# Kernel optimization log

Measured on AMD Instinct MI355X. Metric: run time of the kernel, lower is better.

## Reference

```python
import jax, jax.numpy as jnp
import numpy as np

NEG_BIG = -1e9


def setup_inputs() -> dict:
    key = jax.random.key(0)
    ks = jax.random.split(key, 6)
    B, Tq, Tv, D, A = 4, 256, 1024, 512, 128
    inputs = jax.random.normal(ks[0], (B, Tv, D), dtype=jnp.float32)
    context = jax.random.normal(ks[1], (B, Tq, D), dtype=jnp.float32)
    mask = jnp.ones((B, Tv), dtype=jnp.int32)  # 1 = valid position
    scale = 1.0 / np.sqrt(D)
    Wk = jax.random.normal(ks[2], (D, A), dtype=jnp.float32) * scale
    bk = jnp.zeros((A,), dtype=jnp.float32)
    Wq = jax.random.normal(ks[3], (D, A), dtype=jnp.float32) * scale
    bq = jnp.zeros((A,), dtype=jnp.float32)
    attn_v = jax.random.normal(ks[4], (A,), dtype=jnp.float32) * (1.0 / np.sqrt(A))
    return {"inputs": inputs, "context": context, "mask": mask,
            "Wk": Wk, "bk": bk, "Wq": Wq, "bq": bq, "attn_v": attn_v}


def reference(inputs, context, mask, Wk, bk, Wq, bq, attn_v):
    # inputs: [B,Tv,D] (keys/values), context: [B,Tq,D] (queries)
    k = jnp.einsum('bvd,da->bva', inputs, Wk) + bk        # [B,Tv,A]
    q = jnp.einsum('bqd,da->bqa', context, Wq) + bq       # [B,Tq,A]
    # additive (Bahdanau) score: sum_a v_a * tanh(q + k)
    t = jnp.tanh(q[:, :, None, :] + k[:, None, :, :])     # [B,Tq,Tv,A]
    scores = jnp.einsum('bqva,a->bqv', t, attn_v)         # [B,Tq,Tv]
    neg = (1.0 - mask.astype(jnp.float32))[:, None, :] * NEG_BIG
    scores = scores + neg
    attn = jax.nn.softmax(scores, axis=-1)                # [B,Tq,Tv]
    return jnp.einsum('bqv,bvd->bqd', attn, inputs)       # [B,Tq,D]
```

## Files before the change

### kernel.cpp

```cpp
#include <hip/hip_runtime.h>
#include <math.h>

#define B   4
#define TQ  256
#define TV  1024
#define D   512
#define A   128

#define LOG2E     1.4426950408889634f
#define TWO_LOG2E 2.8853900817779268f
#define NEG_BIG_F (-1e9f)

#define QBLK (B * TQ / 8)
#define KBLK (B * TV / 8)

__global__ __launch_bounds__(512, 4) void proj_exp_kernel(
    const float* __restrict__ ctx, const float* __restrict__ inp,
    const float* __restrict__ Wq, const float* __restrict__ bq,
    const float* __restrict__ Wk, const float* __restrict__ bk,
    float* __restrict__ Eq, float* __restrict__ EkT) {
  __shared__ float ps[8][8][A];
  __shared__ float es[A][9];

  bool isQ = blockIdx.x < QBLK;
  const float* X; const float* W; const float* bias; int r0;
  if (isQ) { X = ctx; W = Wq; bias = bq; r0 = blockIdx.x * 8; }
  else     { X = inp; W = Wk; bias = bk; r0 = (blockIdx.x - QBLK) * 8; }

  int tid = threadIdx.x;
  int ap = (tid & 63) * 2;
  int g  = tid >> 6;

  int dbase = __builtin_amdgcn_readfirstlane(g * 64);
  const float* Xr = X + (size_t)r0 * D + dbase;
  const float* Wd = W + (size_t)dbase * A + ap;

  float2 acc[8];
#pragma unroll
  for (int j = 0; j < 8; ++j) acc[j] = make_float2(0.f, 0.f);

#pragma unroll 2
  for (int dd = 0; dd < 64; dd += 4) {
    float2 w0 = *(const float2*)(Wd + (size_t)(dd + 0) * A);
    float2 w1 = *(const float2*)(Wd + (size_t)(dd + 1) * A);
    float2 w2 = *(const float2*)(Wd + (size_t)(dd + 2) * A);
    float2 w3 = *(const float2*)(Wd + (size_t)(dd + 3) * A);
    float4 x[8];
#pragma unroll
    for (int j = 0; j < 8; ++j)
      x[j] = *(const float4*)(Xr + (size_t)j * D + dd);
#pragma unroll
    for (int j = 0; j < 8; ++j) {
      acc[j].x = fmaf(x[j].x, w0.x, acc[j].x);
      acc[j].y = fmaf(x[j].x, w0.y, acc[j].y);
      acc[j].x = fmaf(x[j].y, w1.x, acc[j].x);
      acc[j].y = fmaf(x[j].y, w1.y, acc[j].y);
      acc[j].x = fmaf(x[j].z, w2.x, acc[j].x);
      acc[j].y = fmaf(x[j].z, w2.y, acc[j].y);
      acc[j].x = fmaf(x[j].w, w3.x, acc[j].x);
      acc[j].y = fmaf(x[j].w, w3.y, acc[j].y);
    }
  }

#pragma unroll
  for (int j = 0; j < 8; ++j)
    *(float2*)&ps[j][g][ap] = acc[j];
  __syncthreads();

  int j  = tid >> 6;
  int a2 = (tid & 63) * 2;
  float2 s0 = *(const float2*)&ps[j][0][a2];
  float2 s1 = *(const float2*)&ps[j][1][a2];
  float2 s2 = *(const float2*)&ps[j][2][a2];
  float2 s3 = *(const float2*)&ps[j][3][a2];
  float2 s4 = *(const float2*)&ps[j][4][a2];
  float2 s5 = *(const float2*)&ps[j][5][a2];
  float2 s6 = *(const float2*)&ps[j][6][a2];
  float2 s7 = *(const float2*)&ps[j][7][a2];
  float2 bz = *(const float2*)(bias + a2);
  float2 ev;
  ev.x = __builtin_amdgcn_exp2f(
      ((((s0.x + s1.x) + (s2.x + s3.x)) + ((s4.x + s5.x) + (s6.x + s7.x))) + bz.x) * TWO_LOG2E);
  ev.y = __builtin_amdgcn_exp2f(
      ((((s0.y + s1.y) + (s2.y + s3.y)) + ((s4.y + s5.y) + (s6.y + s7.y))) + bz.y) * TWO_LOG2E);

  if (isQ) {
    *(float2*)(Eq + (size_t)(r0 + j) * A + a2) = ev;
  } else {
    es[a2 + 0][j] = ev.x;
    es[a2 + 1][j] = ev.y;
    __syncthreads();
    int b  = r0 >> 10;
    int v0 = r0 & (TV - 1);
    for (int i = tid; i < A * 8; i += 512) {
      int aa = i >> 3, jj = i & 7;
      EkT[((size_t)b * A + aa) * TV + v0 + jj] = es[aa][jj];
    }
  }
}

__global__ __launch_bounds__(512, 4) void score_softmax_kernel(
    const float* __restrict__ Eq, const float* __restrict__ EkT,
    const float* __restrict__ attn_v, const int* __restrict__ mask,
    float* __restrict__ attn) {
  __shared__ float redA[8], redB[8];
  __shared__ float bc[4];

  int tid = threadIdx.x;
  int v0  = (tid & 63) * 2 + (tid >> 6) * 128;
  int xcd = blockIdx.x & 7;
  int grp = blockIdx.x >> 3;
  int b   = xcd & 3;
  int pair = (xcd >> 2) * 64 + grp;
  int r0  = b * TQ + pair * 2;

  const float* eqA = Eq + (size_t)r0 * A;
  const float* eqB = eqA + A;

  float sumV = 0.f;
#pragma unroll 16
  for (int i = 0; i < A; ++i) sumV += attn_v[i];

  const float* ekb = EkT + (size_t)b * A * TV + v0;
  float2 tA = make_float2(0.f, 0.f);
  float2 tB = make_float2(0.f, 0.f);

  float2 p00 = *(const float2*)(ekb + (size_t)0 * TV);
  float2 p01 = *(const float2*)(ekb + (size_t)1 * TV);
  float2 p02 = *(const float2*)(ekb + (size_t)2 * TV);
  float2 p03 = *(const float2*)(ekb + (size_t)3 * TV);
  float2 p10 = *(const float2*)(ekb + (size_t)4 * TV);
  float2 p11 = *(const float2*)(ekb + (size_t)5 * TV);
  float2 p12 = *(const float2*)(ekb + (size_t)6 * TV);
  float2 p13 = *(const float2*)(ekb + (size_t)7 * TV);

  for (int i = 0; i < A; i += 8) {
    {
      float av0 = attn_v[i + 0], av1 = attn_v[i + 1];
      float av2 = attn_v[i + 2], av3 = attn_v[i + 3];
      float qa0 = eqA[i + 0], qa1 = eqA[i + 1], qa2 = eqA[i + 2], qa3 = eqA[i + 3];
      float qb0 = eqB[i + 0], qb1 = eqB[i + 1], qb2 = eqB[i + 2], qb3 = eqB[i + 3];

      tA.x = fmaf(av0, __builtin_amdgcn_rcpf(fmaf(p00.x, qa0, 1.f)), tA.x);
      tA.y = fmaf(av0, __builtin_amdgcn_rcpf(fmaf(p00.y, qa0, 1.f)), tA.y);
      tB.x = fmaf(av0, __builtin_amdgcn_rcpf(fmaf(p00.x, qb0, 1.f)), tB.x);
      tB.y = fmaf(av0, __builtin_amdgcn_rcpf(fmaf(p00.y, qb0, 1.f)), tB.y);

      tA.x = fmaf(av1, __builtin_amdgcn_rcpf(fmaf(p01.x, qa1, 1.f)), tA.x);
      tA.y = fmaf(av1, __builtin_amdgcn_rcpf(fmaf(p01.y, qa1, 1.f)), tA.y);
      tB.x = fmaf(av1, __builtin_amdgcn_rcpf(fmaf(p01.x, qb1, 1.f)), tB.x);
      tB.y = fmaf(av1, __builtin_amdgcn_rcpf(fmaf(p01.y, qb1, 1.f)), tB.y);

      tA.x = fmaf(av2, __builtin_amdgcn_rcpf(fmaf(p02.x, qa2, 1.f)), tA.x);
      tA.y = fmaf(av2, __builtin_amdgcn_rcpf(fmaf(p02.y, qa2, 1.f)), tA.y);
      tB.x = fmaf(av2, __builtin_amdgcn_rcpf(fmaf(p02.x, qb2, 1.f)), tB.x);
      tB.y = fmaf(av2, __builtin_amdgcn_rcpf(fmaf(p02.y, qb2, 1.f)), tB.y);

      tA.x = fmaf(av3, __builtin_amdgcn_rcpf(fmaf(p03.x, qa3, 1.f)), tA.x);
      tA.y = fmaf(av3, __builtin_amdgcn_rcpf(fmaf(p03.y, qa3, 1.f)), tA.y);
      tB.x = fmaf(av3, __builtin_amdgcn_rcpf(fmaf(p03.x, qb3, 1.f)), tB.x);
      tB.y = fmaf(av3, __builtin_amdgcn_rcpf(fmaf(p03.y, qb3, 1.f)), tB.y);
    }
    p00 = *(const float2*)(ekb + (size_t)(i + 8) * TV);
    p01 = *(const float2*)(ekb + (size_t)(i + 9) * TV);
    p02 = *(const float2*)(ekb + (size_t)(i + 10) * TV);
    p03 = *(const float2*)(ekb + (size_t)(i + 11) * TV);

    {
      float av0 = attn_v[i + 4], av1 = attn_v[i + 5];
      float av2 = attn_v[i + 6], av3 = attn_v[i + 7];
      float qa0 = eqA[i + 4], qa1 = eqA[i + 5], qa2 = eqA[i + 6], qa3 = eqA[i + 7];
      float qb0 = eqB[i + 4], qb1 = eqB[i + 5], qb2 = eqB[i + 6], qb3 = eqB[i + 7];

      tA.x = fmaf(av0, __builtin_amdgcn_rcpf(fmaf(p10.x, qa0, 1.f)), tA.x);
      tA.y = fmaf(av0, __builtin_amdgcn_rcpf(fmaf(p10.y, qa0, 1.f)), tA.y);
      tB.x = fmaf(av0, __builtin_amdgcn_rcpf(fmaf(p10.x, qb0, 1.f)), tB.x);
      tB.y = fmaf(av0, __builtin_amdgcn_rcpf(fmaf(p10.y, qb0, 1.f)), tB.y);

      tA.x = fmaf(av1, __builtin_amdgcn_rcpf(fmaf(p11.x, qa1, 1.f)), tA.x);
      tA.y = fmaf(av1, __builtin_amdgcn_rcpf(fmaf(p11.y, qa1, 1.f)), tA.y);
      tB.x = fmaf(av1, __builtin_amdgcn_rcpf(fmaf(p11.x, qb1, 1.f)), tB.x);
      tB.y = fmaf(av1, __builtin_amdgcn_rcpf(fmaf(p11.y, qb1, 1.f)), tB.y);

      tA.x = fmaf(av2, __builtin_amdgcn_rcpf(fmaf(p12.x, qa2, 1.f)), tA.x);
      tA.y = fmaf(av2, __builtin_amdgcn_rcpf(fmaf(p12.y, qa2, 1.f)), tA.y);
      tB.x = fmaf(av2, __builtin_amdgcn_rcpf(fmaf(p12.x, qb2, 1.f)), tB.x);
      tB.y = fmaf(av2, __builtin_amdgcn_rcpf(fmaf(p12.y, qb2, 1.f)), tB.y);

      tA.x = fmaf(av3, __builtin_amdgcn_rcpf(fmaf(p13.x, qa3, 1.f)), tA.x);
      tA.y = fmaf(av3, __builtin_amdgcn_rcpf(fmaf(p13.y, qa3, 1.f)), tA.y);
      tB.x = fmaf(av3, __builtin_amdgcn_rcpf(fmaf(p13.x, qb3, 1.f)), tB.x);
      tB.y = fmaf(av3, __builtin_amdgcn_rcpf(fmaf(p13.y, qb3, 1.f)), tB.y);
    }
    p10 = *(const float2*)(ekb + (size_t)(i + 12) * TV);
    p11 = *(const float2*)(ekb + (size_t)(i + 13) * TV);
    p12 = *(const float2*)(ekb + (size_t)(i + 14) * TV);
    p13 = *(const float2*)(ekb + (size_t)(i + 15) * TV);
  }

  int2 mk = *(const int2*)(mask + b * TV + v0);
  float mkx = (1.f - (float)mk.x) * NEG_BIG_F;
  float mky = (1.f - (float)mk.y) * NEG_BIG_F;
  float2 sA, sB;
  sA.x = sumV - 2.f * tA.x + mkx;
  sA.y = sumV - 2.f * tA.y + mky;
  sB.x = sumV - 2.f * tB.x + mkx;
  sB.y = sumV - 2.f * tB.y + mky;

  float mA = fmaxf(sA.x, sA.y);
  float mB = fmaxf(sB.x, sB.y);
  for (int off = 32; off > 0; off >>= 1) {
    mA = fmaxf(mA, __shfl_down(mA, off, 64));
    mB = fmaxf(mB, __shfl_down(mB, off, 64));
  }
  int w = tid >> 6;
  if ((tid & 63) == 0) { redA[w] = mA; redB[w] = mB; }
  __syncthreads();
  if (tid == 0) {
    float a = redA[0], bm = redB[0];
#pragma unroll
    for (int i = 1; i < 8; ++i) { a = fmaxf(a, redA[i]); bm = fmaxf(bm, redB[i]); }
    bc[0] = a; bc[1] = bm;
  }
  __syncthreads();
  float MA = bc[0], MB = bc[1];

  float2 eAv, eBv;
  eAv.x = __builtin_amdgcn_exp2f((sA.x - MA) * LOG2E);
  eAv.y = __builtin_amdgcn_exp2f((sA.y - MA) * LOG2E);
  eBv.x = __builtin_amdgcn_exp2f((sB.x - MB) * LOG2E);
  eBv.y = __builtin_amdgcn_exp2f((sB.y - MB) * LOG2E);
  float lA = eAv.x + eAv.y;
  float lB = eBv.x + eBv.y;
  for (int off = 32; off > 0; off >>= 1) {
    lA += __shfl_down(lA, off, 64);
    lB += __shfl_down(lB, off, 64);
  }
  __syncthreads();
  if ((tid & 63) == 0) { redA[w] = lA; redB[w] = lB; }
  __syncthreads();
  if (tid == 0) {
    float a = 0.f, bs = 0.f;
#pragma unroll
    for (int i = 0; i < 8; ++i) { a += redA[i]; bs += redB[i]; }
    bc[2] = a; bc[3] = bs;
  }
  __syncthreads();
  float iA = 1.f / bc[2];
  float iB = 1.f / bc[3];

  *(float2*)(attn + (size_t)r0 * TV + v0) =
      make_float2(eAv.x * iA, eAv.y * iA);
  *(float2*)(attn + (size_t)(r0 + 1) * TV + v0) =
      make_float2(eBv.x * iB, eBv.y * iB);
}

__global__ __launch_bounds__(512, 4) void pv_kernel(
    const float* __restrict__ attn, const float* __restrict__ X,
    float* __restrict__ out) {
  __shared__ float lds[8 * 1024];
  int gsl = blockIdx.x & 15;
  int b   = gsl & 3;
  int dt  = gsl >> 2;
  int qt  = blockIdx.x >> 4;
  int q0  = b * TQ + qt * 8;
  int tid  = threadIdx.x;
  int w    = tid >> 6;
  int lane = tid & 63;
  int col  = lane & 31;
  int qh   = lane >> 5;
  int d0 = dt * 128 + col * 4;

  {
    const float4* src = (const float4*)(attn + (size_t)q0 * TV);
    float4* dst = (float4*)lds;
    for (int i = tid; i < 8 * 256; i += 512) dst[i] = src[i];
  }
  __syncthreads();

  float4 acc[4];
#pragma unroll
  for (int j = 0; j < 4; ++j) acc[j] = make_float4(0.f, 0.f, 0.f, 0.f);

  int vbase = w * 128;
  const float* Xb = X + ((size_t)b * TV + vbase) * D + d0;
  const float* arow = &lds[(qh * 4) * 1024 + vbase];

  float4 xc0 = *(const float4*)(Xb + (size_t)0 * D);
  float4 xc1 = *(const float4*)(Xb + (size_t)1 * D);
  float4 xc2 = *(const float4*)(Xb + (size_t)2 * D);
  float4 xc3 = *(const float4*)(Xb + (size_t)3 * D);

  for (int vi = 0; vi < 128; vi += 4) {
    float4 xn0, xn1, xn2, xn3;
    if (vi < 124) {
      const float* Xn = Xb + (size_t)(vi + 4) * D;
      xn0 = *(const float4*)(Xn + (size_t)0 * D);
      xn1 = *(const float4*)(Xn + (size_t)1 * D);
      xn2 = *(const float4*)(Xn + (size_t)2 * D);
      xn3 = *(const float4*)(Xn + (size_t)3 * D);
    }
#pragma unroll
    for (int j = 0; j < 4; ++j) {
      float4 av = *(const float4*)(arow + j * 1024 + vi);
      acc[j].x = fmaf(av.x, xc0.x, acc[j].x);
      acc[j].y = fmaf(av.x, xc0.y, acc[j].y);
      acc[j].z = fmaf(av.x, xc0.z, acc[j].z);
      acc[j].w = fmaf(av.x, xc0.w, acc[j].w);
      acc[j].x = fmaf(av.y, xc1.x, acc[j].x);
      acc[j].y = fmaf(av.y, xc1.y, acc[j].y);
      acc[j].z = fmaf(av.y, xc1.z, acc[j].z);
      acc[j].w = fmaf(av.y, xc1.w, acc[j].w);
      acc[j].x = fmaf(av.z, xc2.x, acc[j].x);
      acc[j].y = fmaf(av.z, xc2.y, acc[j].y);
      acc[j].z = fmaf(av.z, xc2.z, acc[j].z);
      acc[j].w = fmaf(av.z, xc2.w, acc[j].w);
      acc[j].x = fmaf(av.w, xc3.x, acc[j].x);
      acc[j].y = fmaf(av.w, xc3.y, acc[j].y);
      acc[j].z = fmaf(av.w, xc3.z, acc[j].z);
      acc[j].w = fmaf(av.w, xc3.w, acc[j].w);
    }
    xc0 = xn0; xc1 = xn1; xc2 = xn2; xc3 = xn3;
  }

  __syncthreads();

  {
    float4* pat = (float4*)lds + (size_t)w * 256;
#pragma unroll
    for (int j = 0; j < 4; ++j)
      pat[(qh * 4 + j) * 32 + col] = acc[j];
  }
  __syncthreads();

  if (tid < 256) {
    int row = tid >> 5;
    int c   = tid & 31;
    const float4* p = (const float4*)lds + tid;
    float4 r = p[0];
#pragma unroll
    for (int i = 1; i < 8; ++i) {
      float4 t = p[(size_t)i * 256];
      r.x += t.x; r.y += t.y; r.z += t.z; r.w += t.w;
    }
    *(float4*)(out + (size_t)(q0 + row) * D + dt * 128 + c * 4) = r;
  }
}

extern "C" void kernel_launch(void* const* d_in, const int* in_sizes, int n_in,
                              void* d_out, int out_size, void* d_ws, size_t ws_size,
                              hipStream_t stream) {
  const float* inputs  = (const float*)d_in[0];
  const float* context = (const float*)d_in[1];
  const int*   mask    = (const int*)d_in[2];
  const float* Wk      = (const float*)d_in[3];
  const float* bk      = (const float*)d_in[4];
  const float* Wq      = (const float*)d_in[5];
  const float* bq      = (const float*)d_in[6];
  const float* attn_v  = (const float*)d_in[7];
  float* out = (float*)d_out;

  float* Eq   = (float*)d_ws;
  float* EkT  = Eq + B * TQ * A;
  float* attn = EkT + (size_t)B * A * TV;

  proj_exp_kernel<<<QBLK + KBLK, 512, 0, stream>>>(context, inputs, Wq, bq,
                                                   Wk, bk, Eq, EkT);
  score_softmax_kernel<<<B * TQ / 2, 512, 0, stream>>>(Eq, EkT, attn_v, mask,
                                                       attn);
  pv_kernel<<<512, 512, 0, stream>>>(attn, inputs, out);
}
```

Measured before the change: 136.6 us.

## Fuse projection, score-softmax and PV into one cooperative kernel with grid syncs

```diff
diff --git a/kernel.cpp b/kernel.cpp
--- a/kernel.cpp
+++ b/kernel.cpp
@@ -1,5 +1,8 @@
 #include <hip/hip_runtime.h>
+#include <hip/hip_cooperative_groups.h>
 #include <math.h>
+
+namespace cg = cooperative_groups;
 
 #define B   4
 #define TQ  256
@@ -13,6 +16,384 @@
 
 #define QBLK (B * TQ / 8)
 #define KBLK (B * TV / 8)
+
+__global__ __launch_bounds__(512, 4) void fused_kernel(
+    const float* __restrict__ ctx, const float* __restrict__ inp,
+    const float* __restrict__ Wq, const float* __restrict__ bq,
+    const float* __restrict__ Wk, const float* __restrict__ bk,
+    const float* __restrict__ attn_v, const int* __restrict__ mask,
+    float* __restrict__ Eq, float* __restrict__ EkT,
+    float* __restrict__ attn, float* __restrict__ out) {
+  __shared__ float lds[8 * 1024];
+  __shared__ float es[A][9];
+  __shared__ float redA[8], redB[8];
+  __shared__ float bc[4];
+
+  int tid = threadIdx.x;
+  int g   = tid >> 6;
+  int ap  = (tid & 63) * 2;
+  float (*ps)[8][A] = (float (*)[8][A])lds;
+
+  int dbase = __builtin_amdgcn_readfirstlane(g * 64);
+
+  {
+    int r0 = blockIdx.x * 8;
+    const float* Xr = inp + (size_t)r0 * D + dbase;
+    const float* Wd = Wk + (size_t)dbase * A + ap;
+
+    float2 acc[8];
+#pragma unroll
+    for (int j = 0; j < 8; ++j) acc[j] = make_float2(0.f, 0.f);
+
+#pragma unroll 2
+    for (int dd = 0; dd < 64; dd += 4) {
+      float2 w0 = *(const float2*)(Wd + (size_t)(dd + 0) * A);
+      float2 w1 = *(const float2*)(Wd + (size_t)(dd + 1) * A);
+      float2 w2 = *(const float2*)(Wd + (size_t)(dd + 2) * A);
+      float2 w3 = *(const float2*)(Wd + (size_t)(dd + 3) * A);
+      float4 x[8];
+#pragma unroll
+      for (int j = 0; j < 8; ++j)
+        x[j] = *(const float4*)(Xr + (size_t)j * D + dd);
+#pragma unroll
+      for (int j = 0; j < 8; ++j) {
+        acc[j].x = fmaf(x[j].x, w0.x, acc[j].x);
+        acc[j].y = fmaf(x[j].x, w0.y, acc[j].y);
+        acc[j].x = fmaf(x[j].y, w1.x, acc[j].x);
+        acc[j].y = fmaf(x[j].y, w1.y, acc[j].y);
+        acc[j].x = fmaf(x[j].z, w2.x, acc[j].x);
+        acc[j].y = fmaf(x[j].z, w2.y, acc[j].y);
+        acc[j].x = fmaf(x[j].w, w3.x, acc[j].x);
+        acc[j].y = fmaf(x[j].w, w3.y, acc[j].y);
+      }
+    }
+
+#pragma unroll
+    for (int j = 0; j < 8; ++j)
+      *(float2*)&ps[j][g][ap] = acc[j];
+    __syncthreads();
+
+    int j  = tid >> 6;
+    int a2 = (tid & 63) * 2;
+    float2 s0 = *(const float2*)&ps[j][0][a2];
+    float2 s1 = *(const float2*)&ps[j][1][a2];
+    float2 s2 = *(const float2*)&ps[j][2][a2];
+    float2 s3 = *(const float2*)&ps[j][3][a2];
+    float2 s4 = *(const float2*)&ps[j][4][a2];
+    float2 s5 = *(const float2*)&ps[j][5][a2];
+    float2 s6 = *(const float2*)&ps[j][6][a2];
+    float2 s7 = *(const float2*)&ps[j][7][a2];
+    float2 bz = *(const float2*)(bk + a2);
+    float2 ev;
+    ev.x = __builtin_amdgcn_exp2f(
+        ((((s0.x + s1.x) + (s2.x + s3.x)) + ((s4.x + s5.x) + (s6.x + s7.x))) + bz.x) * TWO_LOG2E);
+    ev.y = __builtin_amdgcn_exp2f(
+        ((((s0.y + s1.y) + (s2.y + s3.y)) + ((s4.y + s5.y) + (s6.y + s7.y))) + bz.y) * TWO_LOG2E);
+
+    es[a2 + 0][j] = ev.x;
+    es[a2 + 1][j] = ev.y;
+    __syncthreads();
+
+    int b  = r0 >> 10;
+    int v0 = r0 & (TV - 1);
+    for (int i = tid; i < A * 8; i += 512) {
+      int aa = i >> 3, jj = i & 7;
+      EkT[((size_t)b * A + aa) * TV + v0 + jj] = es[aa][jj];
+    }
+  }
+
+  {
+    int r0 = blockIdx.x * 2;
+    const float* Xr = ctx + (size_t)r0 * D + dbase;
+    const float* Wd = Wq + (size_t)dbase * A + ap;
+
+    float2 a0 = make_float2(0.f, 0.f);
+    float2 a1 = make_float2(0.f, 0.f);
+
+#pragma unroll 4
+    for (int dd = 0; dd < 64; dd += 4) {
+      float2 w0 = *(const float2*)(Wd + (size_t)(dd + 0) * A);
+      float2 w1 = *(const float2*)(Wd + (size_t)(dd + 1) * A);
+      float2 w2 = *(const float2*)(Wd + (size_t)(dd + 2) * A);
+      float2 w3 = *(const float2*)(Wd + (size_t)(dd + 3) * A);
+      float4 x0 = *(const float4*)(Xr + (size_t)0 * D + dd);
+      float4 x1 = *(const float4*)(Xr + (size_t)1 * D + dd);
+      a0.x = fmaf(x0.x, w0.x, a0.x);  a0.y = fmaf(x0.x, w0.y, a0.y);
+      a0.x = fmaf(x0.y, w1.x, a0.x);  a0.y = fmaf(x0.y, w1.y, a0.y);
+      a0.x = fmaf(x0.z, w2.x, a0.x);  a0.y = fmaf(x0.z, w2.y, a0.y);
+      a0.x = fmaf(x0.w, w3.x, a0.x);  a0.y = fmaf(x0.w, w3.y, a0.y);
+      a1.x = fmaf(x1.x, w0.x, a1.x);  a1.y = fmaf(x1.x, w0.y, a1.y);
+      a1.x = fmaf(x1.y, w1.x, a1.x);  a1.y = fmaf(x1.y, w1.y, a1.y);
+      a1.x = fmaf(x1.z, w2.x, a1.x);  a1.y = fmaf(x1.z, w2.y, a1.y);
+      a1.x = fmaf(x1.w, w3.x, a1.x);  a1.y = fmaf(x1.w, w3.y, a1.y);
+    }
+
+    *(float2*)&ps[0][g][ap] = a0;
+    *(float2*)&ps[1][g][ap] = a1;
+    __syncthreads();
+
+    if (tid < 128) {
+      int j  = tid >> 6;
+      int a2 = (tid & 63) * 2;
+      float2 s0 = *(const float2*)&ps[j][0][a2];
+      float2 s1 = *(const float2*)&ps[j][1][a2];
+      float2 s2 = *(const float2*)&ps[j][2][a2];
+      float2 s3 = *(const float2*)&ps[j][3][a2];
+      float2 s4 = *(const float2*)&ps[j][4][a2];
+      float2 s5 = *(const float2*)&ps[j][5][a2];
+      float2 s6 = *(const float2*)&ps[j][6][a2];
+      float2 s7 = *(const float2*)&ps[j][7][a2];
+      float2 bz = *(const float2*)(bq + a2);
+      float2 ev;
+      ev.x = __builtin_amdgcn_exp2f(
+          ((((s0.x + s1.x) + (s2.x + s3.x)) + ((s4.x + s5.x) + (s6.x + s7.x))) + bz.x) * TWO_LOG2E);
+      ev.y = __builtin_amdgcn_exp2f(
+          ((((s0.y + s1.y) + (s2.y + s3.y)) + ((s4.y + s5.y) + (s6.y + s7.y))) + bz.y) * TWO_LOG2E);
+      *(float2*)(Eq + (size_t)(r0 + j) * A + a2) = ev;
+    }
+  }
+
+  cg::this_grid().sync();
+
+  {
+    int v0  = (tid & 63) * 2 + (tid >> 6) * 128;
+    int xcd = blockIdx.x & 7;
+    int grp = blockIdx.x >> 3;
+    int b   = xcd & 3;
+    int pair = (xcd >> 2) * 64 + grp;
+    int r0  = b * TQ + pair * 2;
+
+    const float* eqA = Eq + (size_t)r0 * A;
+    const float* eqB = eqA + A;
+
+    float sumV = 0.f;
+#pragma unroll 16
+    for (int i = 0; i < A; ++i) sumV += attn_v[i];
+
+    const float* ekb = EkT + (size_t)b * A * TV + v0;
+    float2 tA = make_float2(0.f, 0.f);
+    float2 tB = make_float2(0.f, 0.f);
+
+    float2 p00 = *(const float2*)(ekb + (size_t)0 * TV);
+    float2 p01 = *(const float2*)(ekb + (size_t)1 * TV);
+    float2 p02 = *(const float2*)(ekb + (size_t)2 * TV);
+    float2 p03 = *(const float2*)(ekb + (size_t)3 * TV);
+    float2 p10 = *(const float2*)(ekb + (size_t)4 * TV);
+    float2 p11 = *(const float2*)(ekb + (size_t)5 * TV);
+    float2 p12 = *(const float2*)(ekb + (size_t)6 * TV);
+    float2 p13 = *(const float2*)(ekb + (size_t)7 * TV);
+
+    for (int i = 0; i < A; i += 8) {
+      {
+        float av0 = attn_v[i + 0], av1 = attn_v[i + 1];
+        float av2 = attn_v[i + 2], av3 = attn_v[i + 3];
+        float qa0 = eqA[i + 0], qa1 = eqA[i + 1], qa2 = eqA[i + 2], qa3 = eqA[i + 3];
+        float qb0 = eqB[i + 0], qb1 = eqB[i + 1], qb2 = eqB[i + 2], qb3 = eqB[i + 3];
+
+        tA.x = fmaf(av0, __builtin_amdgcn_rcpf(fmaf(p00.x, qa0, 1.f)), tA.x);
+        tA.y = fmaf(av0, __builtin_amdgcn_rcpf(fmaf(p00.y, qa0, 1.f)), tA.y);
+        tB.x = fmaf(av0, __builtin_amdgcn_rcpf(fmaf(p00.x, qb0, 1.f)), tB.x);
+        tB.y = fmaf(av0, __builtin_amdgcn_rcpf(fmaf(p00.y, qb0, 1.f)), tB.y);
+
+        tA.x = fmaf(av1, __builtin_amdgcn_rcpf(fmaf(p01.x, qa1, 1.f)), tA.x);
+        tA.y = fmaf(av1, __builtin_amdgcn_rcpf(fmaf(p01.y, qa1, 1.f)), tA.y);
+        tB.x = fmaf(av1, __builtin_amdgcn_rcpf(fmaf(p01.x, qb1, 1.f)), tB.x);
+        tB.y = fmaf(av1, __builtin_amdgcn_rcpf(fmaf(p01.y, qb1, 1.f)), tB.y);
+
+        tA.x = fmaf(av2, __builtin_amdgcn_rcpf(fmaf(p02.x, qa2, 1.f)), tA.x);
+        tA.y = fmaf(av2, __builtin_amdgcn_rcpf(fmaf(p02.y, qa2, 1.f)), tA.y);
+        tB.x = fmaf(av2, __builtin_amdgcn_rcpf(fmaf(p02.x, qb2, 1.f)), tB.x);
+        tB.y = fmaf(av2, __builtin_amdgcn_rcpf(fmaf(p02.y, qb2, 1.f)), tB.y);
+
+        tA.x = fmaf(av3, __builtin_amdgcn_rcpf(fmaf(p03.x, qa3, 1.f)), tA.x);
+        tA.y = fmaf(av3, __builtin_amdgcn_rcpf(fmaf(p03.y, qa3, 1.f)), tA.y);
+        tB.x = fmaf(av3, __builtin_amdgcn_rcpf(fmaf(p03.x, qb3, 1.f)), tB.x);
+        tB.y = fmaf(av3, __builtin_amdgcn_rcpf(fmaf(p03.y, qb3, 1.f)), tB.y);
+      }
+      p00 = *(const float2*)(ekb + (size_t)(i + 8) * TV);
+      p01 = *(const float2*)(ekb + (size_t)(i + 9) * TV);
+      p02 = *(const float2*)(ekb + (size_t)(i + 10) * TV);
+      p03 = *(const float2*)(ekb + (size_t)(i + 11) * TV);
+
+      {
+        float av0 = attn_v[i + 4], av1 = attn_v[i + 5];
+        float av2 = attn_v[i + 6], av3 = attn_v[i + 7];
+        float qa0 = eqA[i + 4], qa1 = eqA[i + 5], qa2 = eqA[i + 6], qa3 = eqA[i + 7];
+        float qb0 = eqB[i + 4], qb1 = eqB[i + 5], qb2 = eqB[i + 6], qb3 = eqB[i + 7];
+
+        tA.x = fmaf(av0, __builtin_amdgcn_rcpf(fmaf(p10.x, qa0, 1.f)), tA.x);
+        tA.y = fmaf(av0, __builtin_amdgcn_rcpf(fmaf(p10.y, qa0, 1.f)), tA.y);
+        tB.x = fmaf(av0, __builtin_amdgcn_rcpf(fmaf(p10.x, qb0, 1.f)), tB.x);
+        tB.y = fmaf(av0, __builtin_amdgcn_rcpf(fmaf(p10.y, qb0, 1.f)), tB.y);
+
+        tA.x = fmaf(av1, __builtin_amdgcn_rcpf(fmaf(p11.x, qa1, 1.f)), tA.x);
+        tA.y = fmaf(av1, __builtin_amdgcn_rcpf(fmaf(p11.y, qa1, 1.f)), tA.y);
+        tB.x = fmaf(av1, __builtin_amdgcn_rcpf(fmaf(p11.x, qb1, 1.f)), tB.x);
+        tB.y = fmaf(av1, __builtin_amdgcn_rcpf(fmaf(p11.y, qb1, 1.f)), tB.y);
+
+        tA.x = fmaf(av2, __builtin_amdgcn_rcpf(fmaf(p12.x, qa2, 1.f)), tA.x);
+        tA.y = fmaf(av2, __builtin_amdgcn_rcpf(fmaf(p12.y, qa2, 1.f)), tA.y);
+        tB.x = fmaf(av2, __builtin_amdgcn_rcpf(fmaf(p12.x, qb2, 1.f)), tB.x);
+        tB.y = fmaf(av2, __builtin_amdgcn_rcpf(fmaf(p12.y, qb2, 1.f)), tB.y);
+
+        tA.x = fmaf(av3, __builtin_amdgcn_rcpf(fmaf(p13.x, qa3, 1.f)), tA.x);
+        tA.y = fmaf(av3, __builtin_amdgcn_rcpf(fmaf(p13.y, qa3, 1.f)), tA.y);
+        tB.x = fmaf(av3, __builtin_amdgcn_rcpf(fmaf(p13.x, qb3, 1.f)), tB.x);
+        tB.y = fmaf(av3, __builtin_amdgcn_rcpf(fmaf(p13.y, qb3, 1.f)), tB.y);
+      }
+      p10 = *(const float2*)(ekb + (size_t)(i + 12) * TV);
+      p11 = *(const float2*)(ekb + (size_t)(i + 13) * TV);
+      p12 = *(const float2*)(ekb + (size_t)(i + 14) * TV);
+      p13 = *(const float2*)(ekb + (size_t)(i + 15) * TV);
+    }
+
+    int2 mk = *(const int2*)(mask + b * TV + v0);
+    float mkx = (1.f - (float)mk.x) * NEG_BIG_F;
+    float mky = (1.f - (float)mk.y) * NEG_BIG_F;
+    float2 sA, sB;
+    sA.x = sumV - 2.f * tA.x + mkx;
+    sA.y = sumV - 2.f * tA.y + mky;
+    sB.x = sumV - 2.f * tB.x + mkx;
+    sB.y = sumV - 2.f * tB.y + mky;
+
+    float mA = fmaxf(sA.x, sA.y);
+    float mB = fmaxf(sB.x, sB.y);
+    for (int off = 32; off > 0; off >>= 1) {
+      mA = fmaxf(mA, __shfl_down(mA, off, 64));
+      mB = fmaxf(mB, __shfl_down(mB, off, 64));
+    }
+    int w = tid >> 6;
+    if ((tid & 63) == 0) { redA[w] = mA; redB[w] = mB; }
+    __syncthreads();
+    if (tid == 0) {
+      float a = redA[0], bm = redB[0];
+#pragma unroll
+      for (int i = 1; i < 8; ++i) { a = fmaxf(a, redA[i]); bm = fmaxf(bm, redB[i]); }
+      bc[0] = a; bc[1] = bm;
+    }
+    __syncthreads();
+    float MA = bc[0], MB = bc[1];
+
+    float2 eAv, eBv;
+    eAv.x = __builtin_amdgcn_exp2f((sA.x - MA) * LOG2E);
+    eAv.y = __builtin_amdgcn_exp2f((sA.y - MA) * LOG2E);
+    eBv.x = __builtin_amdgcn_exp2f((sB.x - MB) * LOG2E);
+    eBv.y = __builtin_amdgcn_exp2f((sB.y - MB) * LOG2E);
+    float lA = eAv.x + eAv.y;
+    float lB = eBv.x + eBv.y;
+    for (int off = 32; off > 0; off >>= 1) {
+      lA += __shfl_down(lA, off, 64);
+      lB += __shfl_down(lB, off, 64);
+    }
+    __syncthreads();
+    if ((tid & 63) == 0) { redA[w] = lA; redB[w] = lB; }
+    __syncthreads();
+    if (tid == 0) {
+      float a = 0.f, bs = 0.f;
+#pragma unroll
+      for (int i = 0; i < 8; ++i) { a += redA[i]; bs += redB[i]; }
+      bc[2] = a; bc[3] = bs;
+    }
+    __syncthreads();
+    float iA = 1.f / bc[2];
+    float iB = 1.f / bc[3];
+
+    *(float2*)(attn + (size_t)r0 * TV + v0) =
+        make_float2(eAv.x * iA, eAv.y * iA);
+    *(float2*)(attn + (size_t)(r0 + 1) * TV + v0) =
+        make_float2(eBv.x * iB, eBv.y * iB);
+  }
+
+  cg::this_grid().sync();
+
+  {
+    int gsl = blockIdx.x & 15;
+    int b   = gsl & 3;
+    int dt  = gsl >> 2;
+    int qt  = blockIdx.x >> 4;
+    int q0  = b * TQ + qt * 8;
+    int w    = tid >> 6;
+    int lane = tid & 63;
+    int col  = lane & 31;
+    int qh   = lane >> 5;
+    int d0 = dt * 128 + col * 4;
+
+    {
+      const float4* src = (const float4*)(attn + (size_t)q0 * TV);
+      float4* dst = (float4*)lds;
+      for (int i = tid; i < 8 * 256; i += 512) dst[i] = src[i];
+    }
+    __syncthreads();
+
+    float4 acc[4];
+#pragma unroll
+    for (int j = 0; j < 4; ++j) acc[j] = make_float4(0.f, 0.f, 0.f, 0.f);
+
+    int vbase = w * 128;
+    const float* Xb = inp + ((size_t)b * TV + vbase) * D + d0;
+    const float* arow = &lds[(qh * 4) * 1024 + vbase];
+
+    float4 xc0 = *(const float4*)(Xb + (size_t)0 * D);
+    float4 xc1 = *(const float4*)(Xb + (size_t)1 * D);
+    float4 xc2 = *(const float4*)(Xb + (size_t)2 * D);
+    float4 xc3 = *(const float4*)(Xb + (size_t)3 * D);
+
+    for (int vi = 0; vi < 128; vi += 4) {
+      float4 xn0, xn1, xn2, xn3;
+      if (vi < 124) {
+        const float* Xn = Xb + (size_t)(vi + 4) * D;
+        xn0 = *(const float4*)(Xn + (size_t)0 * D);
+        xn1 = *(const float4*)(Xn + (size_t)1 * D);
+        xn2 = *(const float4*)(Xn + (size_t)2 * D);
+        xn3 = *(const float4*)(Xn + (size_t)3 * D);
+      }
+#pragma unroll
+      for (int j = 0; j < 4; ++j) {
+        float4 av = *(const float4*)(arow + j * 1024 + vi);
+        acc[j].x = fmaf(av.x, xc0.x, acc[j].x);
+        acc[j].y = fmaf(av.x, xc0.y, acc[j].y);
+        acc[j].z = fmaf(av.x, xc0.z, acc[j].z);
+        acc[j].w = fmaf(av.x, xc0.w, acc[j].w);
+        acc[j].x = fmaf(av.y, xc1.x, acc[j].x);
+        acc[j].y = fmaf(av.y, xc1.y, acc[j].y);
+        acc[j].z = fmaf(av.y, xc1.z, acc[j].z);
+        acc[j].w = fmaf(av.y, xc1.w, acc[j].w);
+        acc[j].x = fmaf(av.z, xc2.x, acc[j].x);
+        acc[j].y = fmaf(av.z, xc2.y, acc[j].y);
+        acc[j].z = fmaf(av.z, xc2.z, acc[j].z);
+        acc[j].w = fmaf(av.z, xc2.w, acc[j].w);
+        acc[j].x = fmaf(av.w, xc3.x, acc[j].x);
+        acc[j].y = fmaf(av.w, xc3.y, acc[j].y);
+        acc[j].z = fmaf(av.w, xc3.z, acc[j].z);
+        acc[j].w = fmaf(av.w, xc3.w, acc[j].w);
+      }
+      xc0 = xn0; xc1 = xn1; xc2 = xn2; xc3 = xn3;
+    }
+
+    __syncthreads();
+
+    {
+      float4* pat = (float4*)lds + (size_t)w * 256;
+#pragma unroll
+      for (int j = 0; j < 4; ++j)
+        pat[(qh * 4 + j) * 32 + col] = acc[j];
+    }
+    __syncthreads();
+
+    if (tid < 256) {
+      int row = tid >> 5;
+      int c   = tid & 31;
+      const float4* p = (const float4*)lds + tid;
+      float4 r = p[0];
+#pragma unroll
+      for (int i = 1; i < 8; ++i) {
+        float4 t = p[(size_t)i * 256];
+        r.x += t.x; r.y += t.y; r.z += t.z; r.w += t.w;
+      }
+      *(float4*)(out + (size_t)(q0 + row) * D + dt * 128 + c * 4) = r;
+    }
+  }
+}
 
 __global__ __launch_bounds__(512, 4) void proj_exp_kernel(
     const float* __restrict__ ctx, const float* __restrict__ inp,
@@ -125,77 +506,45 @@
   float2 tA = make_float2(0.f, 0.f);
   float2 tB = make_float2(0.f, 0.f);
 
-  float2 p00 = *(const float2*)(ekb + (size_t)0 * TV);
-  float2 p01 = *(const float2*)(ekb + (size_t)1 * TV);
-  float2 p02 = *(const float2*)(ekb + (size_t)2 * TV);
-  float2 p03 = *(const float2*)(ekb + (size_t)3 * TV);
-  float2 p10 = *(const float2*)(ekb + (size_t)4 * TV);
-  float2 p11 = *(const float2*)(ekb + (size_t)5 * TV);
-  float2 p12 = *(const float2*)(ekb + (size_t)6 * TV);
-  float2 p13 = *(const float2*)(ekb + (size_t)7 * TV);
-
-  for (int i = 0; i < A; i += 8) {
-    {
-      float av0 = attn_v[i + 0], av1 = attn_v[i + 1];
-      float av2 = attn_v[i + 2], av3 = attn_v[i + 3];
-      float qa0 = eqA[i + 0], qa1 = eqA[i + 1], qa2 = eqA[i + 2], qa3 = eqA[i + 3];
-      float qb0 = eqB[i + 0], qb1 = eqB[i + 1], qb2 = eqB[i + 2], qb3 = eqB[i + 3];
-
-      tA.x = fmaf(av0, __builtin_amdgcn_rcpf(fmaf(p00.x, qa0, 1.f)), tA.x);
-      tA.y = fmaf(av0, __builtin_amdgcn_rcpf(fmaf(p00.y, qa0, 1.f)), tA.y);
-      tB.x = fmaf(av0, __builtin_amdgcn_rcpf(fmaf(p00.x, qb0, 1.f)), tB.x);
-      tB.y = fmaf(av0, __builtin_amdgcn_rcpf(fmaf(p00.y, qb0, 1.f)), tB.y);
-
-      tA.x = fmaf(av1, __builtin_amdgcn_rcpf(fmaf(p01.x, qa1, 1.f)), tA.x);
-      tA.y = fmaf(av1, __builtin_amdgcn_rcpf(fmaf(p01.y, qa1, 1.f)), tA.y);
-      tB.x = fmaf(av1, __builtin_amdgcn_rcpf(fmaf(p01.x, qb1, 1.f)), tB.x);
-      tB.y = fmaf(av1, __builtin_amdgcn_rcpf(fmaf(p01.y, qb1, 1.f)), tB.y);
-
-      tA.x = fmaf(av2, __builtin_amdgcn_rcpf(fmaf(p02.x, qa2, 1.f)), tA.x);
-      tA.y = fmaf(av2, __builtin_amdgcn_rcpf(fmaf(p02.y, qa2, 1.f)), tA.y);
-      tB.x = fmaf(av2, __builtin_amdgcn_rcpf(fmaf(p02.x, qb2, 1.f)), tB.x);
-      tB.y = fmaf(av2, __builtin_amdgcn_rcpf(fmaf(p02.y, qb2, 1.f)), tB.y);
-
-      tA.x = fmaf(av3, __builtin_amdgcn_rcpf(fmaf(p03.x, qa3, 1.f)), tA.x);
-      tA.y = fmaf(av3, __builtin_amdgcn_rcpf(fmaf(p03.y, qa3, 1.f)), tA.y);
-      tB.x = fmaf(av3, __builtin_amdgcn_rcpf(fmaf(p03.x, qb3, 1.f)), tB.x);
-      tB.y = fmaf(av3, __builtin_amdgcn_rcpf(fmaf(p03.y, qb3, 1.f)), tB.y);
-    }
-    p00 = *(const float2*)(ekb + (size_t)(i + 8) * TV);
-    p01 = *(const float2*)(ekb + (size_t)(i + 9) * TV);
-    p02 = *(const float2*)(ekb + (size_t)(i + 10) * TV);
-    p03 = *(const float2*)(ekb + (size_t)(i + 11) * TV);
-
-    {
-      float av0 = attn_v[i + 4], av1 = attn_v[i + 5];
-      float av2 = attn_v[i + 6], av3 = attn_v[i + 7];
-      float qa0 = eqA[i + 4], qa1 = eqA[i + 5], qa2 = eqA[i + 6], qa3 = eqA[i + 7];
-      float qb0 = eqB[i + 4], qb1 = eqB[i + 5], qb2 = eqB[i + 6], qb3 = eqB[i + 7];
-
-      tA.x = fmaf(av0, __builtin_amdgcn_rcpf(fmaf(p10.x, qa0, 1.f)), tA.x);
-      tA.y = fmaf(av0, __builtin_amdgcn_rcpf(fmaf(p10.y, qa0, 1.f)), tA.y);
-      tB.x = fmaf(av0, __builtin_amdgcn_rcpf(fmaf(p10.x, qb0, 1.f)), tB.x);
-      tB.y = fmaf(av0, __builtin_amdgcn_rcpf(fmaf(p10.y, qb0, 1.f)), tB.y);
-
-      tA.x = fmaf(av1, __builtin_amdgcn_rcpf(fmaf(p11.x, qa1, 1.f)), tA.x);
-      tA.y = fmaf(av1, __builtin_amdgcn_rcpf(fmaf(p11.y, qa1, 1.f)), tA.y);
-      tB.x = fmaf(av1, __builtin_amdgcn_rcpf(fmaf(p11.x, qb1, 1.f)), tB.x);
-      tB.y = fmaf(av1, __builtin_amdgcn_rcpf(fmaf(p11.y, qb1, 1.f)), tB.y);
-
-      tA.x = fmaf(av2, __builtin_amdgcn_rcpf(fmaf(p12.x, qa2, 1.f)), tA.x);
-      tA.y = fmaf(av2, __builtin_amdgcn_rcpf(fmaf(p12.y, qa2, 1.f)), tA.y);
-      tB.x = fmaf(av2, __builtin_amdgcn_rcpf(fmaf(p12.x, qb2, 1.f)), tB.x);
-      tB.y = fmaf(av2, __builtin_amdgcn_rcpf(fmaf(p12.y, qb2, 1.f)), tB.y);
-
-      tA.x = fmaf(av3, __builtin_amdgcn_rcpf(fmaf(p13.x, qa3, 1.f)), tA.x);
-      tA.y = fmaf(av3, __builtin_amdgcn_rcpf(fmaf(p13.y, qa3, 1.f)), tA.y);
-      tB.x = fmaf(av3, __builtin_amdgcn_rcpf(fmaf(p13.x, qb3, 1.f)), tB.x);
-      tB.y = fmaf(av3, __builtin_amdgcn_rcpf(fmaf(p13.y, qb3, 1.f)), tB.y);
-    }
-    p10 = *(const float2*)(ekb + (size_t)(i + 12) * TV);
-    p11 = *(const float2*)(ekb + (size_t)(i + 13) * TV);
-    p12 = *(const float2*)(ekb + (size_t)(i + 14) * TV);
-    p13 = *(const float2*)(ekb + (size_t)(i + 15) * TV);
+  float2 c0 = *(const float2*)(ekb + (size_t)0 * TV);
+  float2 c1 = *(const float2*)(ekb + (size_t)1 * TV);
+  float2 c2 = *(const float2*)(ekb + (size_t)2 * TV);
+  float2 c3 = *(const float2*)(ekb + (size_t)3 * TV);
+
+  for (int i = 0; i < A; i += 4) {
+    float2 n0, n1, n2, n3;
+    if (i < A - 4) {
+      n0 = *(const float2*)(ekb + (size_t)(i + 4) * TV);
+      n1 = *(const float2*)(ekb + (size_t)(i + 5) * TV);
+      n2 = *(const float2*)(ekb + (size_t)(i + 6) * TV);
+      n3 = *(const float2*)(ekb + (size_t)(i + 7) * TV);
+    }
+    float av0 = attn_v[i + 0], av1 = attn_v[i + 1];
+    float av2 = attn_v[i + 2], av3 = attn_v[i + 3];
+    float qa0 = eqA[i + 0], qa1 = eqA[i + 1], qa2 = eqA[i + 2], qa3 = eqA[i + 3];
+    float qb0 = eqB[i + 0], qb1 = eqB[i + 1], qb2 = eqB[i + 2], qb3 = eqB[i + 3];
+
+    tA.x = fmaf(av0, __builtin_amdgcn_rcpf(fmaf(c0.x, qa0, 1.f)), tA.x);
+    tA.y = fmaf(av0, __builtin_amdgcn_rcpf(fmaf(c0.y, qa0, 1.f)), tA.y);
+    tB.x = fmaf(av0, __builtin_amdgcn_rcpf(fmaf(c0.x, qb0, 1.f)), tB.x);
+    tB.y = fmaf(av0, __builtin_amdgcn_rcpf(fmaf(c0.y, qb0, 1.f)), tB.y);
+
+    tA.x = fmaf(av1, __builtin_amdgcn_rcpf(fmaf(c1.x, qa1, 1.f)), tA.x);
+    tA.y = fmaf(av1, __builtin_amdgcn_rcpf(fmaf(c1.y, qa1, 1.f)), tA.y);
+    tB.x = fmaf(av1, __builtin_amdgcn_rcpf(fmaf(c1.x, qb1, 1.f)), tB.x);
+    tB.y = fmaf(av1, __builtin_amdgcn_rcpf(fmaf(c1.y, qb1, 1.f)), tB.y);
+
+    tA.x = fmaf(av2, __builtin_amdgcn_rcpf(fmaf(c2.x, qa2, 1.f)), tA.x);
+    tA.y = fmaf(av2, __builtin_amdgcn_rcpf(fmaf(c2.y, qa2, 1.f)), tA.y);
+    tB.x = fmaf(av2, __builtin_amdgcn_rcpf(fmaf(c2.x, qb2, 1.f)), tB.x);
+    tB.y = fmaf(av2, __builtin_amdgcn_rcpf(fmaf(c2.y, qb2, 1.f)), tB.y);
+
+    tA.x = fmaf(av3, __builtin_amdgcn_rcpf(fmaf(c3.x, qa3, 1.f)), tA.x);
+    tA.y = fmaf(av3, __builtin_amdgcn_rcpf(fmaf(c3.y, qa3, 1.f)), tA.y);
+    tB.x = fmaf(av3, __builtin_amdgcn_rcpf(fmaf(c3.x, qb3, 1.f)), tB.x);
+    tB.y = fmaf(av3, __builtin_amdgcn_rcpf(fmaf(c3.y, qb3, 1.f)), tB.y);
+
+    c0 = n0; c1 = n1; c2 = n2; c3 = n3;
   }
 
   int2 mk = *(const int2*)(mask + b * TV + v0);
@@ -364,9 +713,18 @@
   float* EkT  = Eq + B * TQ * A;
   float* attn = EkT + (size_t)B * A * TV;
 
-  proj_exp_kernel<<<QBLK + KBLK, 512, 0, stream>>>(context, inputs, Wq, bq,
-                                                   Wk, bk, Eq, EkT);
-  score_softmax_kernel<<<B * TQ / 2, 512, 0, stream>>>(Eq, EkT, attn_v, mask,
-                                                       attn);
-  pv_kernel<<<512, 512, 0, stream>>>(attn, inputs, out);
+  void* args[] = {(void*)&context, (void*)&inputs,
+                  (void*)&Wq, (void*)&bq, (void*)&Wk, (void*)&bk,
+                  (void*)&attn_v, (void*)&mask,
+                  (void*)&Eq, (void*)&EkT, (void*)&attn, (void*)&out};
+  hipError_t err = hipLaunchCooperativeKernel(
+      (const void*)fused_kernel, dim3(512), dim3(512), args, 0, stream);
+
+  if (err != hipSuccess) {
+    proj_exp_kernel<<<QBLK + KBLK, 512, 0, stream>>>(context, inputs, Wq, bq,
+                                                     Wk, bk, Eq, EkT);
+    score_softmax_kernel<<<B * TQ / 2, 512, 0, stream>>>(Eq, EkT, attn_v, mask,
+                                                         attn);
+    pv_kernel<<<512, 512, 0, stream>>>(attn, inputs, out);
+  }
 }
```

Measured after the change: 274.4 us. 2.01x slower.

## Score four query rows per block and read attn directly in PV kernel

Applied to the files above, without the earlier changes.

```diff
diff --git a/kernel.cpp b/kernel.cpp
--- a/kernel.cpp
+++ b/kernel.cpp
@@ -99,160 +99,114 @@
   }
 }
 
-__global__ __launch_bounds__(512, 4) void score_softmax_kernel(
+__global__ __launch_bounds__(1024, 4) void score_softmax_kernel(
     const float* __restrict__ Eq, const float* __restrict__ EkT,
     const float* __restrict__ attn_v, const int* __restrict__ mask,
     float* __restrict__ attn) {
-  __shared__ float redA[8], redB[8];
-  __shared__ float bc[4];
+  __shared__ float red[4][16];
+  __shared__ float bc[8];
 
   int tid = threadIdx.x;
-  int v0  = (tid & 63) * 2 + (tid >> 6) * 128;
+  int v0  = tid;
   int xcd = blockIdx.x & 7;
-  int grp = blockIdx.x >> 3;
   int b   = xcd & 3;
-  int pair = (xcd >> 2) * 64 + grp;
-  int r0  = b * TQ + pair * 2;
-
-  const float* eqA = Eq + (size_t)r0 * A;
-  const float* eqB = eqA + A;
+  int quad = (xcd >> 2) * 32 + (blockIdx.x >> 3);
+  int r0  = b * TQ + quad * 4;
+
+  const float* eq0 = Eq + (size_t)(r0 + 0) * A;
+  const float* eq1 = Eq + (size_t)(r0 + 1) * A;
+  const float* eq2 = Eq + (size_t)(r0 + 2) * A;
+  const float* eq3 = Eq + (size_t)(r0 + 3) * A;
 
   float sumV = 0.f;
 #pragma unroll 16
   for (int i = 0; i < A; ++i) sumV += attn_v[i];
 
   const float* ekb = EkT + (size_t)b * A * TV + v0;
-  float2 tA = make_float2(0.f, 0.f);
-  float2 tB = make_float2(0.f, 0.f);
-
-  float2 p00 = *(const float2*)(ekb + (size_t)0 * TV);
-  float2 p01 = *(const float2*)(ekb + (size_t)1 * TV);
-  float2 p02 = *(const float2*)(ekb + (size_t)2 * TV);
-  float2 p03 = *(const float2*)(ekb + (size_t)3 * TV);
-  float2 p10 = *(const float2*)(ekb + (size_t)4 * TV);
-  float2 p11 = *(const float2*)(ekb + (size_t)5 * TV);
-  float2 p12 = *(const float2*)(ekb + (size_t)6 * TV);
-  float2 p13 = *(const float2*)(ekb + (size_t)7 * TV);
-
-  for (int i = 0; i < A; i += 8) {
-    {
-      float av0 = attn_v[i + 0], av1 = attn_v[i + 1];
-      float av2 = attn_v[i + 2], av3 = attn_v[i + 3];
-      float qa0 = eqA[i + 0], qa1 = eqA[i + 1], qa2 = eqA[i + 2], qa3 = eqA[i + 3];
-      float qb0 = eqB[i + 0], qb1 = eqB[i + 1], qb2 = eqB[i + 2], qb3 = eqB[i + 3];
-
-      tA.x = fmaf(av0, __builtin_amdgcn_rcpf(fmaf(p00.x, qa0, 1.f)), tA.x);
-      tA.y = fmaf(av0, __builtin_amdgcn_rcpf(fmaf(p00.y, qa0, 1.f)), tA.y);
-      tB.x = fmaf(av0, __builtin_amdgcn_rcpf(fmaf(p00.x, qb0, 1.f)), tB.x);
-      tB.y = fmaf(av0, __builtin_amdgcn_rcpf(fmaf(p00.y, qb0, 1.f)), tB.y);
-
-      tA.x = fmaf(av1, __builtin_amdgcn_rcpf(fmaf(p01.x, qa1, 1.f)), tA.x);
-      tA.y = fmaf(av1, __builtin_amdgcn_rcpf(fmaf(p01.y, qa1, 1.f)), tA.y);
-      tB.x = fmaf(av1, __builtin_amdgcn_rcpf(fmaf(p01.x, qb1, 1.f)), tB.x);
-      tB.y = fmaf(av1, __builtin_amdgcn_rcpf(fmaf(p01.y, qb1, 1.f)), tB.y);
-
-      tA.x = fmaf(av2, __builtin_amdgcn_rcpf(fmaf(p02.x, qa2, 1.f)), tA.x);
-      tA.y = fmaf(av2, __builtin_amdgcn_rcpf(fmaf(p02.y, qa2, 1.f)), tA.y);
-      tB.x = fmaf(av2, __builtin_amdgcn_rcpf(fmaf(p02.x, qb2, 1.f)), tB.x);
-      tB.y = fmaf(av2, __builtin_amdgcn_rcpf(fmaf(p02.y, qb2, 1.f)), tB.y);
-
-      tA.x = fmaf(av3, __builtin_amdgcn_rcpf(fmaf(p03.x, qa3, 1.f)), tA.x);
-      tA.y = fmaf(av3, __builtin_amdgcn_rcpf(fmaf(p03.y, qa3, 1.f)), tA.y);
-      tB.x = fmaf(av3, __builtin_amdgcn_rcpf(fmaf(p03.x, qb3, 1.f)), tB.x);
-      tB.y = fmaf(av3, __builtin_amdgcn_rcpf(fmaf(p03.y, qb3, 1.f)), tB.y);
-    }
-    p00 = *(const float2*)(ekb + (size_t)(i + 8) * TV);
-    p01 = *(const float2*)(ekb + (size_t)(i + 9) * TV);
-    p02 = *(const float2*)(ekb + (size_t)(i + 10) * TV);
-    p03 = *(const float2*)(ekb + (size_t)(i + 11) * TV);
-
-    {
-      float av0 = attn_v[i + 4], av1 = attn_v[i + 5];
-      float av2 = attn_v[i + 6], av3 = attn_v[i + 7];
-      float qa0 = eqA[i + 4], qa1 = eqA[i + 5], qa2 = eqA[i + 6], qa3 = eqA[i + 7];
-      float qb0 = eqB[i + 4], qb1 = eqB[i + 5], qb2 = eqB[i + 6], qb3 = eqB[i + 7];
-
-      tA.x = fmaf(av0, __builtin_amdgcn_rcpf(fmaf(p10.x, qa0, 1.f)), tA.x);
-      tA.y = fmaf(av0, __builtin_amdgcn_rcpf(fmaf(p10.y, qa0, 1.f)), tA.y);
-      tB.x = fmaf(av0, __builtin_amdgcn_rcpf(fmaf(p10.x, qb0, 1.f)), tB.x);
-      tB.y = fmaf(av0, __builtin_amdgcn_rcpf(fmaf(p10.y, qb0, 1.f)), tB.y);
-
-      tA.x = fmaf(av1, __builtin_amdgcn_rcpf(fmaf(p11.x, qa1, 1.f)), tA.x);
-      tA.y = fmaf(av1, __builtin_amdgcn_rcpf(fmaf(p11.y, qa1, 1.f)), tA.y);
-      tB.x = fmaf(av1, __builtin_amdgcn_rcpf(fmaf(p11.x, qb1, 1.f)), tB.x);
-      tB.y = fmaf(av1, __builtin_amdgcn_rcpf(fmaf(p11.y, qb1, 1.f)), tB.y);
-
-      tA.x = fmaf(av2, __builtin_amdgcn_rcpf(fmaf(p12.x, qa2, 1.f)), tA.x);
-      tA.y = fmaf(av2, __builtin_amdgcn_rcpf(fmaf(p12.y, qa2, 1.f)), tA.y);
-      tB.x = fmaf(av2, __builtin_amdgcn_rcpf(fmaf(p12.x, qb2, 1.f)), tB.x);
-      tB.y = fmaf(av2, __builtin_amdgcn_rcpf(fmaf(p12.y, qb2, 1.f)), tB.y);
-
-      tA.x = fmaf(av3, __builtin_amdgcn_rcpf(fmaf(p13.x, qa3, 1.f)), tA.x);
-      tA.y = fmaf(av3, __builtin_amdgcn_rcpf(fmaf(p13.y, qa3, 1.f)), tA.y);
-      tB.x = fmaf(av3, __builtin_amdgcn_rcpf(fmaf(p13.x, qb3, 1.f)), tB.x);
-      tB.y = fmaf(av3, __builtin_amdgcn_rcpf(fmaf(p13.y, qb3, 1.f)), tB.y);
-    }
-    p10 = *(const float2*)(ekb + (size_t)(i + 12) * TV);
-    p11 = *(const float2*)(ekb + (size_t)(i + 13) * TV);
-    p12 = *(const float2*)(ekb + (size_t)(i + 14) * TV);
-    p13 = *(const float2*)(ekb + (size_t)(i + 15) * TV);
-  }
-
-  int2 mk = *(const int2*)(mask + b * TV + v0);
-  float mkx = (1.f - (float)mk.x) * NEG_BIG_F;
-  float mky = (1.f - (float)mk.y) * NEG_BIG_F;
-  float2 sA, sB;
-  sA.x = sumV - 2.f * tA.x + mkx;
-  sA.y = sumV - 2.f * tA.y + mky;
-  sB.x = sumV - 2.f * tB.x + mkx;
-  sB.y = sumV - 2.f * tB.y + mky;
-
-  float mA = fmaxf(sA.x, sA.y);
-  float mB = fmaxf(sB.x, sB.y);
+  float t[4] = {0.f, 0.f, 0.f, 0.f};
+
+  float c[4], n[4];
+#pragma unroll
+  for (int aa = 0; aa < 4; ++aa) c[aa] = ekb[(size_t)aa * TV];
+
+  for (int i = 0; i < A; i += 4) {
+    if (i < A - 4) {
+#pragma unroll
+      for (int aa = 0; aa < 4; ++aa) n[aa] = ekb[(size_t)(i + 4 + aa) * TV];
+    }
+#pragma unroll
+    for (int aa = 0; aa < 4; ++aa) {
+      float av = attn_v[i + aa];
+      float q0v = eq0[i + aa], q1v = eq1[i + aa];
+      float q2v = eq2[i + aa], q3v = eq3[i + aa];
+      t[0] = fmaf(av, __builtin_amdgcn_rcpf(fmaf(c[aa], q0v, 1.f)), t[0]);
+      t[1] = fmaf(av, __builtin_amdgcn_rcpf(fmaf(c[aa], q1v, 1.f)), t[1]);
+      t[2] = fmaf(av, __builtin_amdgcn_rcpf(fmaf(c[aa], q2v, 1.f)), t[2]);
+      t[3] = fmaf(av, __builtin_amdgcn_rcpf(fmaf(c[aa], q3v, 1.f)), t[3]);
+    }
+#pragma unroll
+    for (int aa = 0; aa < 4; ++aa) c[aa] = n[aa];
+  }
+
+  int mk = mask[b * TV + v0];
+  float mkv = (1.f - (float)mk) * NEG_BIG_F;
+  float s[4];
+#pragma unroll
+  for (int r = 0; r < 4; ++r) s[r] = sumV - 2.f * t[r] + mkv;
+
+  float m[4];
+#pragma unroll
+  for (int r = 0; r < 4; ++r) m[r] = s[r];
   for (int off = 32; off > 0; off >>= 1) {
-    mA = fmaxf(mA, __shfl_down(mA, off, 64));
-    mB = fmaxf(mB, __shfl_down(mB, off, 64));
+#pragma unroll
+    for (int r = 0; r < 4; ++r) m[r] = fmaxf(m[r], __shfl_down(m[r], off, 64));
   }
   int w = tid >> 6;
-  if ((tid & 63) == 0) { redA[w] = mA; redB[w] = mB; }
-  __syncthreads();
-  if (tid == 0) {
-    float a = redA[0], bm = redB[0];
-#pragma unroll
-    for (int i = 1; i < 8; ++i) { a = fmaxf(a, redA[i]); bm = fmaxf(bm, redB[i]); }
-    bc[0] = a; bc[1] = bm;
-  }
-  __syncthreads();
-  float MA = bc[0], MB = bc[1];
-
-  float2 eAv, eBv;
-  eAv.x = __builtin_amdgcn_exp2f((sA.x - MA) * LOG2E);
-  eAv.y = __builtin_amdgcn_exp2f((sA.y - MA) * LOG2E);
-  eBv.x = __builtin_amdgcn_exp2f((sB.x - MB) * LOG2E);
-  eBv.y = __builtin_amdgcn_exp2f((sB.y - MB) * LOG2E);
-  float lA = eAv.x + eAv.y;
-  float lB = eBv.x + eBv.y;
+  if ((tid & 63) == 0) {
+#pragma unroll
+    for (int r = 0; r < 4; ++r) red[r][w] = m[r];
+  }
+  __syncthreads();
+  if (tid < 4) {
+    float a = red[tid][0];
+#pragma unroll
+    for (int i = 1; i < 16; ++i) a = fmaxf(a, red[tid][i]);
+    bc[tid] = a;
+  }
+  __syncthreads();
+  float M0 = bc[0], M1 = bc[1], M2 = bc[2], M3 = bc[3];
+
+  float e[4];
+  e[0] = __builtin_amdgcn_exp2f((s[0] - M0) * LOG2E);
+  e[1] = __builtin_amdgcn_exp2f((s[1] - M1) * LOG2E);
+  e[2] = __builtin_amdgcn_exp2f((s[2] - M2) * LOG2E);
+  e[3] = __builtin_amdgcn_exp2f((s[3] - M3) * LOG2E);
+  float l[4];
+#pragma unroll
+  for (int r = 0; r < 4; ++r) l[r] = e[r];
   for (int off = 32; off > 0; off >>= 1) {
-    lA += __shfl_down(lA, off, 64);
-    lB += __shfl_down(lB, off, 64);
-  }
-  __syncthreads();
-  if ((tid & 63) == 0) { redA[w] = lA; redB[w] = lB; }
-  __syncthreads();
-  if (tid == 0) {
-    float a = 0.f, bs = 0.f;
-#pragma unroll
-    for (int i = 0; i < 8; ++i) { a += redA[i]; bs += redB[i]; }
-    bc[2] = a; bc[3] = bs;
-  }
-  __syncthreads();
-  float iA = 1.f / bc[2];
-  float iB = 1.f / bc[3];
-
-  *(float2*)(attn + (size_t)r0 * TV + v0) =
-      make_float2(eAv.x * iA, eAv.y * iA);
-  *(float2*)(attn + (size_t)(r0 + 1) * TV + v0) =
-      make_float2(eBv.x * iB, eBv.y * iB);
+#pragma unroll
+    for (int r = 0; r < 4; ++r) l[r] += __shfl_down(l[r], off, 64);
+  }
+  __syncthreads();
+  if ((tid & 63) == 0) {
+#pragma unroll
+    for (int r = 0; r < 4; ++r) red[r][w] = l[r];
+  }
+  __syncthreads();
+  if (tid < 4) {
+    float a = 0.f;
+#pragma unroll
+    for (int i = 0; i < 16; ++i) a += red[tid][i];
+    bc[4 + tid] = a;
+  }
+  __syncthreads();
+  float i0 = 1.f / bc[4], i1 = 1.f / bc[5], i2 = 1.f / bc[6], i3 = 1.f / bc[7];
+
+  attn[(size_t)(r0 + 0) * TV + v0] = e[0] * i0;
+  attn[(size_t)(r0 + 1) * TV + v0] = e[1] * i1;
+  attn[(size_t)(r0 + 2) * TV + v0] = e[2] * i2;
+  attn[(size_t)(r0 + 3) * TV + v0] = e[3] * i3;
 }
 
 __global__ __launch_bounds__(512, 4) void pv_kernel(
@@ -271,25 +225,22 @@
   int qh   = lane >> 5;
   int d0 = dt * 128 + col * 4;
 
-  {
-    const float4* src = (const float4*)(attn + (size_t)q0 * TV);
-    float4* dst = (float4*)lds;
-    for (int i = tid; i < 8 * 256; i += 512) dst[i] = src[i];
-  }
-  __syncthreads();
-
   float4 acc[4];
 #pragma unroll
   for (int j = 0; j < 4; ++j) acc[j] = make_float4(0.f, 0.f, 0.f, 0.f);
 
   int vbase = w * 128;
   const float* Xb = X + ((size_t)b * TV + vbase) * D + d0;
-  const float* arow = &lds[(qh * 4) * 1024 + vbase];
+  const float* arow = attn + (size_t)(q0 + qh * 4) * TV + vbase;
 
   float4 xc0 = *(const float4*)(Xb + (size_t)0 * D);
   float4 xc1 = *(const float4*)(Xb + (size_t)1 * D);
   float4 xc2 = *(const float4*)(Xb + (size_t)2 * D);
   float4 xc3 = *(const float4*)(Xb + (size_t)3 * D);
+  float4 ac[4], an[4];
+#pragma unroll
+  for (int j = 0; j < 4; ++j)
+    ac[j] = *(const float4*)(arow + (size_t)j * TV);
 
   for (int vi = 0; vi < 128; vi += 4) {
     float4 xn0, xn1, xn2, xn3;
@@ -299,10 +250,13 @@
       xn1 = *(const float4*)(Xn + (size_t)1 * D);
       xn2 = *(const float4*)(Xn + (size_t)2 * D);
       xn3 = *(const float4*)(Xn + (size_t)3 * D);
+#pragma unroll
+      for (int j = 0; j < 4; ++j)
+        an[j] = *(const float4*)(arow + (size_t)j * TV + vi + 4);
     }
 #pragma unroll
     for (int j = 0; j < 4; ++j) {
-      float4 av = *(const float4*)(arow + j * 1024 + vi);
+      float4 av = ac[j];
       acc[j].x = fmaf(av.x, xc0.x, acc[j].x);
       acc[j].y = fmaf(av.x, xc0.y, acc[j].y);
       acc[j].z = fmaf(av.x, xc0.z, acc[j].z);
@@ -321,9 +275,9 @@
       acc[j].w = fmaf(av.w, xc3.w, acc[j].w);
     }
     xc0 = xn0; xc1 = xn1; xc2 = xn2; xc3 = xn3;
-  }
-
-  __syncthreads();
+#pragma unroll
+    for (int j = 0; j < 4; ++j) ac[j] = an[j];
+  }
 
   {
     float4* pat = (float4*)lds + (size_t)w * 256;
@@ -366,7 +320,7 @@
 
   proj_exp_kernel<<<QBLK + KBLK, 512, 0, stream>>>(context, inputs, Wq, bq,
                                                    Wk, bk, Eq, EkT);
-  score_softmax_kernel<<<B * TQ / 2, 512, 0, stream>>>(Eq, EkT, attn_v, mask,
-                                                       attn);
+  score_softmax_kernel<<<B * TQ / 4, 1024, 0, stream>>>(Eq, EkT, attn_v, mask,
+                                                        attn);
   pv_kernel<<<512, 512, 0, stream>>>(attn, inputs, out);
 }
```

New measurement: 146.8 us. 1.07x slower.
